# Optimization experiments

Measured on AMD Instinct MI355X. Metric: run time of the kernel, lower is better.

The kernel has to match this reference:

```python
import jax, jax.numpy as jnp
import numpy as np

D = 1024
H = 16
HD = D // H
EPS = 1e-5


def layer_norm(x, g, b):
    mu = jnp.mean(x, axis=-1, keepdims=True)
    var = jnp.var(x, axis=-1, keepdims=True)
    return (x - mu) * jax.lax.rsqrt(var + EPS) * g + b


def setup_inputs() -> dict:
    key = jax.random.key(0)
    ks = jax.random.split(key, 16)
    s = 0.02
    return {
        "x": jax.random.normal(ks[0], (2, 2048, D), jnp.float32),
        "ln1_g": jnp.ones((D,), jnp.float32),
        "ln1_b": jnp.zeros((D,), jnp.float32),
        "Wq": jax.random.normal(ks[1], (D, D), jnp.float32) * s,
        "bq": jnp.zeros((D,), jnp.float32),
        "Wk": jax.random.normal(ks[2], (D, D), jnp.float32) * s,
        "bk": jnp.zeros((D,), jnp.float32),
        "Wv": jax.random.normal(ks[3], (D, D), jnp.float32) * s,
        "bv": jnp.zeros((D,), jnp.float32),
        "Wo": jax.random.normal(ks[4], (D, D), jnp.float32) * s,
        "bo": jnp.zeros((D,), jnp.float32),
        "ln2_g": jnp.ones((D,), jnp.float32),
        "ln2_b": jnp.zeros((D,), jnp.float32),
        "W1": jax.random.normal(ks[5], (D, 4 * D), jnp.float32) * s,
        "b1": jnp.zeros((4 * D,), jnp.float32),
        "W2": jax.random.normal(ks[6], (4 * D, D), jnp.float32) * s,
        "b2": jnp.zeros((D,), jnp.float32),
    }


def reference(x, ln1_g, ln1_b, Wq, bq, Wk, bk, Wv, bv, Wo, bo, ln2_g, ln2_b, W1, b1, W2, b2):
    B, T, _ = x.shape
    # --- attention sub-block (pre-LN) ---
    h = layer_norm(x, ln1_g, ln1_b)
    q = (h @ Wq + bq).reshape(B, T, H, HD).transpose(0, 2, 1, 3)  # [B,H,T,hd]
    k = (h @ Wk + bk).reshape(B, T, H, HD).transpose(0, 2, 1, 3)
    v = (h @ Wv + bv).reshape(B, T, H, HD).transpose(0, 2, 1, 3)
    scores = jnp.einsum("bhqd,bhkd->bhqk", q, k)  # full O(T^2) scores as in source
    causal = jnp.tril(jnp.ones((T, T), bool))
    scores = jnp.where(causal, scores, -jnp.inf)
    w = jax.nn.softmax(scores / np.sqrt(HD), axis=-1)
    ctx = jnp.einsum("bhqk,bhkd->bhqd", w, v)
    ctx = ctx.transpose(0, 2, 1, 3).reshape(B, T, D)
    x = x + (ctx @ Wo + bo)
    # --- MLP sub-block (pre-LN) ---
    h = layer_norm(x, ln2_g, ln2_b)
    h = jax.nn.gelu(h @ W1 + b1, approximate=False)
    x = x + (h @ W2 + b2)
    return x
```

## Files before the change

kernel.cpp:

```cpp
#include <hip/hip_runtime.h>
#include <math.h>


typedef _Float16 half8 __attribute__((ext_vector_type(8)));
typedef _Float16 half4v __attribute__((ext_vector_type(4)));
typedef float floatx4 __attribute__((ext_vector_type(4)));

#define DMODEL 1024
#define SEQT   2048
#define NTOK   4096
#define NHEAD  16
#define HDIM   64

__device__ __forceinline__ void llds16(const _Float16* g, _Float16* l) {
  __builtin_amdgcn_global_load_lds(
      (const __attribute__((address_space(1))) void*)g,
      (__attribute__((address_space(3))) void*)l, 16, 0, 0);
}

__global__ __launch_bounds__(256) void wtrans_kernel(
    const float* __restrict__ Wq, const float* __restrict__ Wk,
    const float* __restrict__ Wv, const float* __restrict__ Wo,
    const float* __restrict__ W1, const float* __restrict__ W2,
    _Float16* __restrict__ wt_base) {
  __shared__ float tilebuf[32][33];
  int id = blockIdx.x;
  const float* src; _Float16* dst; int K, N, t;
  if (id < 4096) {
    int s = id >> 10;
    src = (s == 0) ? Wq : (s == 1) ? Wk : (s == 2) ? Wv : Wo;
    dst = wt_base + (size_t)s * (1024 * 1024);
    K = 1024; N = 1024; t = id & 1023;
  } else if (id < 8192) {
    src = W1; dst = wt_base + (size_t)4 * 1024 * 1024; K = 1024; N = 4096; t = id - 4096;
  } else {
    src = W2; dst = wt_base + (size_t)8 * 1024 * 1024; K = 4096; N = 1024; t = id - 8192;
  }
  int tilesN = N >> 5;
  int tk = t / tilesN, tn = t % tilesN;
  int c = threadIdx.x & 31, r0 = threadIdx.x >> 5;
#pragma unroll
  for (int i = 0; i < 4; ++i) {
    int r = r0 + i * 8;
    tilebuf[r][c] = src[(size_t)(tk * 32 + r) * N + tn * 32 + c];
  }
  __syncthreads();
#pragma unroll
  for (int i = 0; i < 4; ++i) {
    int r = r0 + i * 8;
    dst[(size_t)(tn * 32 + r) * K + tk * 32 + c] = (_Float16)tilebuf[c][r];
  }
}

__global__ __launch_bounds__(256) void ln_kernel(
    const float* __restrict__ x, const float* __restrict__ g,
    const float* __restrict__ b, _Float16* __restrict__ out) {
  int row = blockIdx.x;
  int t = threadIdx.x;
  const float4 xv = ((const float4*)(x + (size_t)row * DMODEL))[t];
  float s = xv.x + xv.y + xv.z + xv.w;
  float s2 = xv.x * xv.x + xv.y * xv.y + xv.z * xv.z + xv.w * xv.w;
#pragma unroll
  for (int off = 32; off; off >>= 1) {
    s += __shfl_down(s, off);
    s2 += __shfl_down(s2, off);
  }
  __shared__ float red[8];
  int wid = t >> 6;
  if ((t & 63) == 0) { red[wid] = s; red[wid + 4] = s2; }
  __syncthreads();
  s = red[0] + red[1] + red[2] + red[3];
  s2 = red[4] + red[5] + red[6] + red[7];
  float mu = s * (1.0f / DMODEL);
  float var = s2 * (1.0f / DMODEL) - mu * mu;
  float rstd = rsqrtf(var + 1e-5f);
  const float4 gv = ((const float4*)g)[t];
  const float4 bv = ((const float4*)b)[t];
  half4v o;
  o[0] = (_Float16)((xv.x - mu) * rstd * gv.x + bv.x);
  o[1] = (_Float16)((xv.y - mu) * rstd * gv.y + bv.y);
  o[2] = (_Float16)((xv.z - mu) * rstd * gv.z + bv.z);
  o[3] = (_Float16)((xv.w - mu) * rstd * gv.w + bv.w);
  *(half4v*)(out + (size_t)row * DMODEL + t * 4) = o;
}

template <int MODE>
__global__ __launch_bounds__(256) void gemm_kernel(
    const _Float16* __restrict__ A, const _Float16* __restrict__ Bt0, int K,
    const float* __restrict__ bias0, const float* __restrict__ bias1,
    const float* __restrict__ bias2, const float* __restrict__ res,
    float* __restrict__ outf, _Float16* __restrict__ outh) {
  constexpr int NT = (MODE == 1) ? 64 : 128;
  constexpr int MI = (NT == 128) ? 4 : 2;
  constexpr int BCH = NT / 64;
  __shared__ __align__(16) _Float16 As[2][128 * 32];
  __shared__ __align__(16) _Float16 Bs[2][NT * 32];
  const int tid = threadIdx.x;
  const int m0 = blockIdx.x * 128;
  const _Float16* Bt;
  const float* bias;
  _Float16* outh_sel = outh;
  int n0, sel = 0;
  if (MODE == 0) {
    sel = blockIdx.y >> 3;
    n0 = (blockIdx.y & 7) * 128;
    Bt = Bt0 + (size_t)sel * (1024 * 1024);
    bias = (sel == 0) ? bias0 : (sel == 1) ? bias1 : bias2;
    outh_sel = outh + (size_t)sel * ((size_t)NTOK * DMODEL);
  } else {
    n0 = blockIdx.y * NT;
    Bt = Bt0;
    bias = bias0;
  }
  const int w = tid >> 6, lane = tid & 63;
  const int l15 = lane & 15, q8 = lane >> 4;
  const int wrow = (NT == 128) ? (w >> 1) * 64 : w * 32;
  const int wcol = (NT == 128) ? (w & 1) * 64 : 0;

  const _Float16* gA[2]; int ldsA[2];
  const _Float16* gB[BCH]; int ldsB[BCH];
#pragma unroll
  for (int i = 0; i < 2; ++i) {
    int c0 = i * 256 + w * 64;
    int idx = c0 + lane;
    int m = idx >> 2, kq = (idx & 3) * 8;
    gA[i] = A + (size_t)(m0 + m) * K + kq;
    ldsA[i] = c0 * 8;
  }
#pragma unroll
  for (int i = 0; i < BCH; ++i) {
    int c0 = i * 256 + w * 64;
    int idx = c0 + lane;
    int m = idx >> 2, kq = (idx & 3) * 8;
    gB[i] = Bt + (size_t)(n0 + m) * K + kq;
    ldsB[i] = c0 * 8;
  }

  auto stage = [&](int buf) {
#pragma unroll
    for (int i = 0; i < 2; ++i) {
      llds16(gA[i], &As[buf][ldsA[i]]);
      gA[i] += 32;
    }
#pragma unroll
    for (int i = 0; i < BCH; ++i) {
      llds16(gB[i], &Bs[buf][ldsB[i]]);
      gB[i] += 32;
    }
  };

  floatx4 acc[MI][4];
#pragma unroll
  for (int i = 0; i < MI; ++i)
#pragma unroll
    for (int j = 0; j < 4; ++j) acc[i][j] = (floatx4){0.f, 0.f, 0.f, 0.f};

  const int nk = K >> 5;
  stage(0);
  __syncthreads();
  for (int t = 0; t < nk; ++t) {
    const int buf = t & 1;
    if (t + 1 < nk) stage(buf ^ 1);
    half8 af[MI], bf[4];
#pragma unroll
    for (int i = 0; i < MI; ++i)
      af[i] = *(const half8*)&As[buf][(wrow + i * 16 + l15) * 32 + q8 * 8];
#pragma unroll
    for (int j = 0; j < 4; ++j)
      bf[j] = *(const half8*)&Bs[buf][(wcol + j * 16 + l15) * 32 + q8 * 8];
#pragma unroll
    for (int i = 0; i < MI; ++i)
#pragma unroll
      for (int j = 0; j < 4; ++j)
        acc[i][j] = __builtin_amdgcn_mfma_f32_16x16x32_f16(af[i], bf[j], acc[i][j], 0, 0, 0);
    __syncthreads();
  }

#pragma unroll
  for (int i = 0; i < MI; ++i) {
    int rowb = m0 + wrow + i * 16 + q8 * 4;
#pragma unroll
    for (int j = 0; j < 4; ++j) {
      int col = n0 + wcol + j * 16 + l15;
      float bval = bias[col];
#pragma unroll
      for (int r = 0; r < 4; ++r) {
        int row = rowb + r;
        float v = acc[i][j][r] + bval;
        if (MODE == 0) {
          int bb = row >> 11, tt = row & 2047;
          int hh = col >> 6, hd = col & 63;
          if (sel == 2)
            outh_sel[((size_t)(bb * NHEAD + hh) * HDIM + hd) * SEQT + tt] = (_Float16)v;
          else
            outh_sel[((size_t)(bb * NHEAD + hh) * SEQT + tt) * HDIM + hd] = (_Float16)v;
        } else if (MODE == 1) {
          v += res[(size_t)row * 1024 + col];
          outf[(size_t)row * 1024 + col] = v;
        } else {
          float z = 1.5957691216f * v * (1.0f + 0.044715f * v * v);
          float gl = v / (1.0f + __expf(-z));
          outh[(size_t)row * 4096 + col] = (_Float16)gl;
        }
      }
    }
  }
}

__global__ __launch_bounds__(256) void attn_kernel(
    const _Float16* __restrict__ q, const _Float16* __restrict__ k,
    const _Float16* __restrict__ vt, _Float16* __restrict__ ctx) {
  __shared__ __align__(16) _Float16 Ks[2][64 * 64];
  __shared__ __align__(16) _Float16 Vs[2][64 * 64];
  __shared__ __align__(16) _Float16 Ps[64 * 72];
  __shared__ float Lpart[4][64];
  const int tid = threadIdx.x;
  const int w = tid >> 6, lane = tid & 63;
  const int l15 = lane & 15, q8 = lane >> 4;
  const int bh = blockIdx.y;
  const int pr = blockIdx.x;
  const size_t base = (size_t)bh * SEQT * HDIM;

  const _Float16* gk0[2]; const _Float16* gv0[2]; int ldsc[2];
#pragma unroll
  for (int i = 0; i < 2; ++i) {
    int c = i * 256 + w * 64 + lane;
    int r = c >> 3, gc = ((c & 7) ^ (r & 7)) * 8;
    gk0[i] = k + base + (size_t)r * HDIM + gc;
    gv0[i] = vt + base + (size_t)r * SEQT + gc;
    ldsc[i] = c * 8;
  }
  auto stage = [&](int kt, int buf) {
#pragma unroll
    for (int i = 0; i < 2; ++i) {
      llds16(gk0[i] + (size_t)kt * (64 * HDIM), &Ks[buf][ldsc[i]]);
      llds16(gv0[i] + kt * 64, &Vs[buf][ldsc[i]]);
    }
  };

  const int rswA = (l15 & 7);
  const int cs0 = (q8 ^ rswA) * 8;
  const int cs1 = ((4 + q8) ^ rswA) * 8;

  int s = 0;
  stage(0, 0);
  __syncthreads();
  for (int ph = 0; ph < 2; ++ph) {
    const int qtile = ph ? 31 - pr : pr;
    const int ntile = qtile + 1;
    half8 bq[4][2];
#pragma unroll
    for (int nt = 0; nt < 4; ++nt) {
      const half8* qp = (const half8*)(q + base + (size_t)(qtile * 64 + nt * 16 + l15) * HDIM);
      bq[nt][0] = qp[q8];
      bq[nt][1] = qp[4 + q8];
    }
    floatx4 acc[4];
#pragma unroll
    for (int j = 0; j < 4; ++j) acc[j] = (floatx4){0.f, 0.f, 0.f, 0.f};
    float lsum[4] = {0.f, 0.f, 0.f, 0.f};

    for (int jt = 0; jt < ntile; ++jt, ++s) {
      const int buf = s & 1;
      if (s + 1 < 33) {
        int sn = s + 1;
        int nkt = (sn <= pr) ? sn : sn - (pr + 1);
        stage(nkt, buf ^ 1);
      }
      half8 ak0 = *(const half8*)&Ks[buf][(w * 16 + l15) * 64 + cs0];
      half8 ak1 = *(const half8*)&Ks[buf][(w * 16 + l15) * 64 + cs1];
      floatx4 sv[4];
#pragma unroll
      for (int nt = 0; nt < 4; ++nt) {
        sv[nt] = __builtin_amdgcn_mfma_f32_16x16x32_f16(ak0, bq[nt][0],
                                                        (floatx4){0.f, 0.f, 0.f, 0.f}, 0, 0, 0);
        sv[nt] = __builtin_amdgcn_mfma_f32_16x16x32_f16(ak1, bq[nt][1], sv[nt], 0, 0, 0);
      }
      const bool diag = (jt == ntile - 1);
#pragma unroll
      for (int nt = 0; nt < 4; ++nt) {
        half4v phv;
#pragma unroll
        for (int r = 0; r < 4; ++r) {
          float p = __expf(sv[nt][r] * 0.125f);
          if (diag) {
            p = (w * 16 + q8 * 4 + r <= nt * 16 + l15) ? p : 0.f;
          }
          lsum[nt] += p;
          phv[r] = (_Float16)p;
        }
        *(half4v*)&Ps[(nt * 16 + l15) * 72 + w * 16 + q8 * 4] = phv;
      }
      __syncthreads();
      half8 ap0 = *(const half8*)&Ps[(w * 16 + l15) * 72 + q8 * 8];
      half8 ap1 = *(const half8*)&Ps[(w * 16 + l15) * 72 + 32 + q8 * 8];
#pragma unroll
      for (int ntd = 0; ntd < 4; ++ntd) {
        half8 bv0 = *(const half8*)&Vs[buf][(ntd * 16 + l15) * 64 + cs0];
        half8 bv1 = *(const half8*)&Vs[buf][(ntd * 16 + l15) * 64 + cs1];
        acc[ntd] = __builtin_amdgcn_mfma_f32_16x16x32_f16(ap0, bv0, acc[ntd], 0, 0, 0);
        acc[ntd] = __builtin_amdgcn_mfma_f32_16x16x32_f16(ap1, bv1, acc[ntd], 0, 0, 0);
      }
      __syncthreads();
    }

#pragma unroll
    for (int nt = 0; nt < 4; ++nt) {
      lsum[nt] += __shfl_xor(lsum[nt], 16);
      lsum[nt] += __shfl_xor(lsum[nt], 32);
      if (q8 == 0) Lpart[w][nt * 16 + l15] = lsum[nt];
    }
    __syncthreads();
    const int b = bh >> 4, h = bh & 15;
#pragma unroll
    for (int r = 0; r < 4; ++r) {
      int qr = w * 16 + q8 * 4 + r;
      float inv = 1.0f / (Lpart[0][qr] + Lpart[1][qr] + Lpart[2][qr] + Lpart[3][qr]);
      int tg = qtile * 64 + qr;
      _Float16* op = ctx + ((size_t)(b * SEQT + tg)) * DMODEL + h * HDIM;
#pragma unroll
      for (int ntd = 0; ntd < 4; ++ntd)
        op[ntd * 16 + l15] = (_Float16)(acc[ntd][r] * inv);
    }
  }
}

extern "C" void kernel_launch(void* const* d_in, const int* in_sizes, int n_in,
                              void* d_out, int out_size, void* d_ws, size_t ws_size,
                              hipStream_t stream) {
  (void)in_sizes; (void)n_in; (void)out_size; (void)ws_size;
  const float* x    = (const float*)d_in[0];
  const float* ln1g = (const float*)d_in[1];
  const float* ln1b = (const float*)d_in[2];
  const float* Wq   = (const float*)d_in[3];
  const float* bq   = (const float*)d_in[4];
  const float* Wk   = (const float*)d_in[5];
  const float* bk   = (const float*)d_in[6];
  const float* Wv   = (const float*)d_in[7];
  const float* bv   = (const float*)d_in[8];
  const float* Wo   = (const float*)d_in[9];
  const float* bo   = (const float*)d_in[10];
  const float* ln2g = (const float*)d_in[11];
  const float* ln2b = (const float*)d_in[12];
  const float* W1   = (const float*)d_in[13];
  const float* b1   = (const float*)d_in[14];
  const float* W2   = (const float*)d_in[15];
  const float* b2   = (const float*)d_in[16];
  float* out = (float*)d_out;

  char* ws = (char*)d_ws;
  _Float16* wt    = (_Float16*)(ws);
  _Float16* h16   = (_Float16*)(ws + ((size_t)24 << 20));
  _Float16* qkv   = (_Float16*)(ws + ((size_t)32 << 20));
  _Float16* ctx16 = (_Float16*)(ws + ((size_t)24 << 20));
  float*    x1    = (float*)   (ws + ((size_t)32 << 20));
  _Float16* h2    = (_Float16*)(ws + ((size_t)48 << 20));
  _Float16* mid   = (_Float16*)(ws + ((size_t)56 << 20));

  const size_t QKV1 = (size_t)NTOK * DMODEL;

  wtrans_kernel<<<12288, 256, 0, stream>>>(Wq, Wk, Wv, Wo, W1, W2, wt);
  ln_kernel<<<NTOK, 256, 0, stream>>>(x, ln1g, ln1b, h16);
  gemm_kernel<0><<<dim3(32, 24), 256, 0, stream>>>(
      h16, wt, 1024, bq, bk, bv, nullptr, nullptr, qkv);
  attn_kernel<<<dim3(16, 32), 256, 0, stream>>>(
      qkv, qkv + QKV1, qkv + 2 * QKV1, ctx16);
  gemm_kernel<1><<<dim3(32, 16), 256, 0, stream>>>(
      ctx16, wt + (size_t)3 * 1024 * 1024, 1024, bo, nullptr, nullptr, x, x1, nullptr);
  ln_kernel<<<NTOK, 256, 0, stream>>>(x1, ln2g, ln2b, h2);
  gemm_kernel<2><<<dim3(32, 32), 256, 0, stream>>>(
      h2, wt + (size_t)4 * 1024 * 1024, 1024, b1, nullptr, nullptr, nullptr, nullptr, mid);
  gemm_kernel<1><<<dim3(32, 16), 256, 0, stream>>>(
      mid, wt + (size_t)8 * 1024 * 1024, 4096, b2, nullptr, nullptr, x1, out, nullptr);
}
```

Baseline: 379.5 us.

## Add dedicated producer wave with 3-stage LDS ring and spin-flag sync in GEMM

```diff
diff --git a/kernel.cpp b/kernel.cpp
--- a/kernel.cpp
+++ b/kernel.cpp
@@ -17,6 +17,9 @@
       (const __attribute__((address_space(1))) void*)g,
       (__attribute__((address_space(3))) void*)l, 16, 0, 0);
 }
+
+#define WAITCNT_VM(n)  ((n & 15) | ((n >> 4) << 14) | 0x0F70)
+#define WAITCNT_LGKM0  (0xC07F)
 
 __global__ __launch_bounds__(256) void wtrans_kernel(
     const float* __restrict__ Wq, const float* __restrict__ Wk,
@@ -85,17 +88,22 @@
 }
 
 template <int MODE>
-__global__ __launch_bounds__(256) void gemm_kernel(
+__global__ __launch_bounds__(320) void gemm_kernel(
     const _Float16* __restrict__ A, const _Float16* __restrict__ Bt0, int K,
     const float* __restrict__ bias0, const float* __restrict__ bias1,
     const float* __restrict__ bias2, const float* __restrict__ res,
     float* __restrict__ outf, _Float16* __restrict__ outh) {
   constexpr int NT = (MODE == 1) ? 64 : 128;
   constexpr int MI = (NT == 128) ? 4 : 2;
-  constexpr int BCH = NT / 64;
-  __shared__ __align__(16) _Float16 As[2][128 * 32];
-  __shared__ __align__(16) _Float16 Bs[2][NT * 32];
+  constexpr int NSTAGE = 3;
+  constexpr int ACH = 8;
+  constexpr int BCH = NT / 16;
+  constexpr int IPT = ACH + BCH;
+  __shared__ __align__(16) _Float16 As[NSTAGE][128 * 32];
+  __shared__ __align__(16) _Float16 Bs[NSTAGE][NT * 32];
+  __shared__ int ready_f, done_f;
   const int tid = threadIdx.x;
+  const int w = tid >> 6, lane = tid & 63;
   const int m0 = blockIdx.x * 128;
   const _Float16* Bt;
   const float* bias;
@@ -112,68 +120,71 @@
     Bt = Bt0;
     bias = bias0;
   }
-  const int w = tid >> 6, lane = tid & 63;
+  if (tid == 0) { ready_f = 0; done_f = 0; }
+  __syncthreads();
+  volatile int* rv = &ready_f;
+  volatile int* dv = &done_f;
+  const int nk = K >> 5;
+
+  if (w == 4) {
+    const int r4 = lane >> 2, c8 = (lane & 3) * 8;
+    const _Float16* gA = A + (size_t)(m0 + r4) * K + c8;
+    const _Float16* gB = Bt + (size_t)(n0 + r4) * K + c8;
+    for (int t = 0; t < nk; ++t) {
+      if (t >= NSTAGE) {
+        const int need = 4 * (t - NSTAGE + 1);
+        while (*dv < need) {}
+      }
+      const int slot = t % NSTAGE;
+      _Float16* la = &As[slot][0];
+      _Float16* lb = &Bs[slot][0];
+#pragma unroll
+      for (int i = 0; i < ACH; ++i)
+        llds16(gA + (size_t)(i * 16) * K, la + i * 512);
+#pragma unroll
+      for (int i = 0; i < BCH; ++i)
+        llds16(gB + (size_t)(i * 16) * K, lb + i * 512);
+      gA += 32; gB += 32;
+      if (t >= 2) {
+        __builtin_amdgcn_s_waitcnt(WAITCNT_VM(2 * IPT));
+        if (lane == 0) *rv = t - 1;
+      }
+    }
+    __builtin_amdgcn_s_waitcnt(WAITCNT_VM(0));
+    if (lane == 0) *rv = nk;
+    return;
+  }
+
   const int l15 = lane & 15, q8 = lane >> 4;
   const int wrow = (NT == 128) ? (w >> 1) * 64 : w * 32;
   const int wcol = (NT == 128) ? (w & 1) * 64 : 0;
 
-  const _Float16* gA[2]; int ldsA[2];
-  const _Float16* gB[BCH]; int ldsB[BCH];
-#pragma unroll
-  for (int i = 0; i < 2; ++i) {
-    int c0 = i * 256 + w * 64;
-    int idx = c0 + lane;
-    int m = idx >> 2, kq = (idx & 3) * 8;
-    gA[i] = A + (size_t)(m0 + m) * K + kq;
-    ldsA[i] = c0 * 8;
-  }
-#pragma unroll
-  for (int i = 0; i < BCH; ++i) {
-    int c0 = i * 256 + w * 64;
-    int idx = c0 + lane;
-    int m = idx >> 2, kq = (idx & 3) * 8;
-    gB[i] = Bt + (size_t)(n0 + m) * K + kq;
-    ldsB[i] = c0 * 8;
-  }
-
-  auto stage = [&](int buf) {
-#pragma unroll
-    for (int i = 0; i < 2; ++i) {
-      llds16(gA[i], &As[buf][ldsA[i]]);
-      gA[i] += 32;
-    }
-#pragma unroll
-    for (int i = 0; i < BCH; ++i) {
-      llds16(gB[i], &Bs[buf][ldsB[i]]);
-      gB[i] += 32;
-    }
-  };
-
   floatx4 acc[MI][4];
 #pragma unroll
   for (int i = 0; i < MI; ++i)
 #pragma unroll
     for (int j = 0; j < 4; ++j) acc[i][j] = (floatx4){0.f, 0.f, 0.f, 0.f};
 
-  const int nk = K >> 5;
-  stage(0);
-  __syncthreads();
   for (int t = 0; t < nk; ++t) {
-    const int buf = t & 1;
-    if (t + 1 < nk) stage(buf ^ 1);
+    while (*rv < t + 1) {}
+    const int slot = t % NSTAGE;
+    const _Float16* as = &As[slot][0];
+    const _Float16* bs = &Bs[slot][0];
     half8 af[MI], bf[4];
 #pragma unroll
     for (int i = 0; i < MI; ++i)
-      af[i] = *(const half8*)&As[buf][(wrow + i * 16 + l15) * 32 + q8 * 8];
+      af[i] = *(const half8*)&as[(wrow + i * 16 + l15) * 32 + q8 * 8];
 #pragma unroll
     for (int j = 0; j < 4; ++j)
-      bf[j] = *(const half8*)&Bs[buf][(wcol + j * 16 + l15) * 32 + q8 * 8];
+      bf[j] = *(const half8*)&bs[(wcol + j * 16 + l15) * 32 + q8 * 8];
+    __builtin_amdgcn_sched_barrier(0);
+    __builtin_amdgcn_s_waitcnt(WAITCNT_LGKM0);
+    if (lane == 0) atomicAdd(&done_f, 1);
 #pragma unroll
     for (int i = 0; i < MI; ++i)
 #pragma unroll
       for (int j = 0; j < 4; ++j)
         acc[i][j] = __builtin_amdgcn_mfma_f32_16x16x32_f16(af[i], bf[j], acc[i][j], 0, 0, 0);
-    __syncthreads();
   }
 
 #pragma unroll
@@ -361,15 +372,15 @@
 
   wtrans_kernel<<<12288, 256, 0, stream>>>(Wq, Wk, Wv, Wo, W1, W2, wt);
   ln_kernel<<<NTOK, 256, 0, stream>>>(x, ln1g, ln1b, h16);
-  gemm_kernel<0><<<dim3(32, 24), 256, 0, stream>>>(
+  gemm_kernel<0><<<dim3(32, 24), 320, 0, stream>>>(
       h16, wt, 1024, bq, bk, bv, nullptr, nullptr, qkv);
   attn_kernel<<<dim3(16, 32), 256, 0, stream>>>(
       qkv, qkv + QKV1, qkv + 2 * QKV1, ctx16);
-  gemm_kernel<1><<<dim3(32, 16), 256, 0, stream>>>(
+  gemm_kernel<1><<<dim3(32, 16), 320, 0, stream>>>(
       ctx16, wt + (size_t)3 * 1024 * 1024, 1024, bo, nullptr, nullptr, x, x1, nullptr);
   ln_kernel<<<NTOK, 256, 0, stream>>>(x1, ln2g, ln2b, h2);
-  gemm_kernel<2><<<dim3(32, 32), 256, 0, stream>>>(
+  gemm_kernel<2><<<dim3(32, 32), 320, 0, stream>>>(
       h2, wt + (size_t)4 * 1024 * 1024, 1024, b1, nullptr, nullptr, nullptr, nullptr, mid);
-  gemm_kernel<1><<<dim3(32, 16), 256, 0, stream>>>(
+  gemm_kernel<1><<<dim3(32, 16), 320, 0, stream>>>(
       mid, wt + (size_t)8 * 1024 * 1024, 4096, b2, nullptr, nullptr, x1, out, nullptr);
 }
```

After: 398.9 us. 1.05x slower.

## Use 4-stage LDS pipeline with vmcnt waits and uniform 128x64 GEMM tiles

Applied to the files above, without the earlier changes.

```diff
diff --git a/kernel.cpp b/kernel.cpp
--- a/kernel.cpp
+++ b/kernel.cpp
@@ -17,6 +17,8 @@
       (const __attribute__((address_space(1))) void*)g,
       (__attribute__((address_space(3))) void*)l, 16, 0, 0);
 }
+
+#define WAITCNT_VM(n)  (((n) & 15) | (((n) >> 4) << 14) | 0x0F70)
 
 __global__ __launch_bounds__(256) void wtrans_kernel(
     const float* __restrict__ Wq, const float* __restrict__ Wk,
@@ -90,35 +92,31 @@
     const float* __restrict__ bias0, const float* __restrict__ bias1,
     const float* __restrict__ bias2, const float* __restrict__ res,
     float* __restrict__ outf, _Float16* __restrict__ outh) {
-  constexpr int NT = (MODE == 1) ? 64 : 128;
-  constexpr int MI = (NT == 128) ? 4 : 2;
-  constexpr int BCH = NT / 64;
-  __shared__ __align__(16) _Float16 As[2][128 * 32];
-  __shared__ __align__(16) _Float16 Bs[2][NT * 32];
+  __shared__ __align__(16) _Float16 As[4][128 * 32];
+  __shared__ __align__(16) _Float16 Bs[4][64 * 32];
   const int tid = threadIdx.x;
+  const int w = tid >> 6, lane = tid & 63;
   const int m0 = blockIdx.x * 128;
   const _Float16* Bt;
   const float* bias;
   _Float16* outh_sel = outh;
   int n0, sel = 0;
   if (MODE == 0) {
-    sel = blockIdx.y >> 3;
-    n0 = (blockIdx.y & 7) * 128;
+    sel = blockIdx.y >> 4;
+    n0 = (blockIdx.y & 15) * 64;
     Bt = Bt0 + (size_t)sel * (1024 * 1024);
     bias = (sel == 0) ? bias0 : (sel == 1) ? bias1 : bias2;
     outh_sel = outh + (size_t)sel * ((size_t)NTOK * DMODEL);
   } else {
-    n0 = blockIdx.y * NT;
+    n0 = blockIdx.y * 64;
     Bt = Bt0;
     bias = bias0;
   }
-  const int w = tid >> 6, lane = tid & 63;
   const int l15 = lane & 15, q8 = lane >> 4;
-  const int wrow = (NT == 128) ? (w >> 1) * 64 : w * 32;
-  const int wcol = (NT == 128) ? (w & 1) * 64 : 0;
+  const int wrow = w * 32;
 
   const _Float16* gA[2]; int ldsA[2];
-  const _Float16* gB[BCH]; int ldsB[BCH];
+  const _Float16* gB; int ldsB;
 #pragma unroll
   for (int i = 0; i < 2; ++i) {
     int c0 = i * 256 + w * 64;
@@ -127,61 +125,64 @@
     gA[i] = A + (size_t)(m0 + m) * K + kq;
     ldsA[i] = c0 * 8;
   }
-#pragma unroll
-  for (int i = 0; i < BCH; ++i) {
-    int c0 = i * 256 + w * 64;
+  {
+    int c0 = w * 64;
     int idx = c0 + lane;
     int m = idx >> 2, kq = (idx & 3) * 8;
-    gB[i] = Bt + (size_t)(n0 + m) * K + kq;
-    ldsB[i] = c0 * 8;
-  }
-
-  auto stage = [&](int buf) {
-#pragma unroll
-    for (int i = 0; i < 2; ++i) {
-      llds16(gA[i], &As[buf][ldsA[i]]);
-      gA[i] += 32;
-    }
-#pragma unroll
-    for (int i = 0; i < BCH; ++i) {
-      llds16(gB[i], &Bs[buf][ldsB[i]]);
-      gB[i] += 32;
-    }
+    gB = Bt + (size_t)(n0 + m) * K + kq;
+    ldsB = c0 * 8;
+  }
+  auto stage = [&](int slot) {
+    llds16(gA[0], &As[slot][ldsA[0]]); gA[0] += 32;
+    llds16(gA[1], &As[slot][ldsA[1]]); gA[1] += 32;
+    llds16(gB, &Bs[slot][ldsB]);       gB += 32;
   };
 
-  floatx4 acc[MI][4];
-#pragma unroll
-  for (int i = 0; i < MI; ++i)
+  floatx4 acc[2][4];
+#pragma unroll
+  for (int i = 0; i < 2; ++i)
 #pragma unroll
     for (int j = 0; j < 4; ++j) acc[i][j] = (floatx4){0.f, 0.f, 0.f, 0.f};
+
+  auto compute = [&](int slot) {
+    const _Float16* as = &As[slot][0];
+    const _Float16* bs = &Bs[slot][0];
+    half8 af[2], bf[4];
+#pragma unroll
+    for (int i = 0; i < 2; ++i)
+      af[i] = *(const half8*)&as[(wrow + i * 16 + l15) * 32 + q8 * 8];
+#pragma unroll
+    for (int j = 0; j < 4; ++j)
+      bf[j] = *(const half8*)&bs[(j * 16 + l15) * 32 + q8 * 8];
+#pragma unroll
+    for (int i = 0; i < 2; ++i)
+#pragma unroll
+      for (int j = 0; j < 4; ++j)
+        acc[i][j] = __builtin_amdgcn_mfma_f32_16x16x32_f16(af[i], bf[j], acc[i][j], 0, 0, 0);
+  };
 
   const int nk = K >> 5;
   stage(0);
-  __syncthreads();
-  for (int t = 0; t < nk; ++t) {
-    const int buf = t & 1;
-    if (t + 1 < nk) stage(buf ^ 1);
-    half8 af[MI], bf[4];
-#pragma unroll
-    for (int i = 0; i < MI; ++i)
-      af[i] = *(const half8*)&As[buf][(wrow + i * 16 + l15) * 32 + q8 * 8];
-#pragma unroll
-    for (int j = 0; j < 4; ++j)
-      bf[j] = *(const half8*)&Bs[buf][(wcol + j * 16 + l15) * 32 + q8 * 8];
-#pragma unroll
-    for (int i = 0; i < MI; ++i)
-#pragma unroll
-      for (int j = 0; j < 4; ++j)
-        acc[i][j] = __builtin_amdgcn_mfma_f32_16x16x32_f16(af[i], bf[j], acc[i][j], 0, 0, 0);
-    __syncthreads();
-  }
-
-#pragma unroll
-  for (int i = 0; i < MI; ++i) {
+  stage(1);
+  for (int t = 0; t < nk - 2; ++t) {
+    stage((t + 2) & 3);
+    __builtin_amdgcn_s_waitcnt(WAITCNT_VM(6));
+    asm volatile("s_barrier" ::: "memory");
+    compute(t & 3);
+  }
+  __builtin_amdgcn_s_waitcnt(WAITCNT_VM(3));
+  asm volatile("s_barrier" ::: "memory");
+  compute((nk - 2) & 3);
+  __builtin_amdgcn_s_waitcnt(WAITCNT_VM(0));
+  asm volatile("s_barrier" ::: "memory");
+  compute((nk - 1) & 3);
+
+#pragma unroll
+  for (int i = 0; i < 2; ++i) {
     int rowb = m0 + wrow + i * 16 + q8 * 4;
 #pragma unroll
     for (int j = 0; j < 4; ++j) {
-      int col = n0 + wcol + j * 16 + l15;
+      int col = n0 + j * 16 + l15;
       float bval = bias[col];
 #pragma unroll
       for (int r = 0; r < 4; ++r) {
@@ -361,14 +362,14 @@
 
   wtrans_kernel<<<12288, 256, 0, stream>>>(Wq, Wk, Wv, Wo, W1, W2, wt);
   ln_kernel<<<NTOK, 256, 0, stream>>>(x, ln1g, ln1b, h16);
-  gemm_kernel<0><<<dim3(32, 24), 256, 0, stream>>>(
+  gemm_kernel<0><<<dim3(32, 48), 256, 0, stream>>>(
       h16, wt, 1024, bq, bk, bv, nullptr, nullptr, qkv);
   attn_kernel<<<dim3(16, 32), 256, 0, stream>>>(
       qkv, qkv + QKV1, qkv + 2 * QKV1, ctx16);
   gemm_kernel<1><<<dim3(32, 16), 256, 0, stream>>>(
       ctx16, wt + (size_t)3 * 1024 * 1024, 1024, bo, nullptr, nullptr, x, x1, nullptr);
   ln_kernel<<<NTOK, 256, 0, stream>>>(x1, ln2g, ln2b, h2);
-  gemm_kernel<2><<<dim3(32, 32), 256, 0, stream>>>(
+  gemm_kernel<2><<<dim3(32, 64), 256, 0, stream>>>(
       h2, wt + (size_t)4 * 1024 * 1024, 1024, b1, nullptr, nullptr, nullptr, nullptr, mid);
   gemm_kernel<1><<<dim3(32, 16), 256, 0, stream>>>(
       mid, wt + (size_t)8 * 1024 * 1024, 4096, b2, nullptr, nullptr, x1, out, nullptr);
```

Measured after the change: 381.0 us. No clear change (+0.4%).
